# Kernel tuning notes

Hardware: AMD Instinct MI355X
Metric: run time of the kernel (lower is better)

## Reference

```python
import jax, jax.numpy as jnp
import numpy as np

C = 128
EPS = 1e-5


def _ln(x, g, b):
    m = jnp.mean(x, axis=-1, keepdims=True)
    v = jnp.mean((x - m) ** 2, axis=-1, keepdims=True)
    return (x - m) * jax.lax.rsqrt(v + EPS) * g + b


def setup_inputs() -> dict:
    key = jax.random.key(0)
    ks = jax.random.split(key, 10)
    B, N = 1, 384
    s = 1.0 / np.sqrt(C)
    inp = {
        "z": jax.random.normal(ks[0], (B, N, N, C), dtype=jnp.float32),
        "ln1_g": jnp.ones((C,), jnp.float32),
        "ln1_b": jnp.zeros((C,), jnp.float32),
        "ln2_g": jnp.ones((C,), jnp.float32),
        "ln2_b": jnp.zeros((C,), jnp.float32),
        "Wa": jax.random.uniform(ks[1], (C, C), jnp.float32, -s, s),
        "ba": jnp.zeros((C,), jnp.float32),
        "Wga": jax.random.uniform(ks[2], (C, C), jnp.float32, -s, s),
        "bga": jnp.zeros((C,), jnp.float32),
        "Wb": jax.random.uniform(ks[3], (C, C), jnp.float32, -s, s),
        "bb": jnp.zeros((C,), jnp.float32),
        "Wgb": jax.random.uniform(ks[4], (C, C), jnp.float32, -s, s),
        "bgb": jnp.zeros((C,), jnp.float32),
        "Wg": jax.random.uniform(ks[5], (C, C), jnp.float32, -s, s),
        "bg": jnp.zeros((C,), jnp.float32),
        "Wo": jax.random.uniform(ks[6], (C, C), jnp.float32, -s, s),
        "bo": jnp.zeros((C,), jnp.float32),
    }
    return inp


def reference(z, ln1_g, ln1_b, ln2_g, ln2_b, Wa, ba, Wga, bga, Wb, bb, Wgb, bgb, Wg, bg, Wo, bo):
    # z: (B, i, j, c)
    zn = _ln(z, ln1_g, ln1_b)
    a = (zn @ Wa + ba) * jax.nn.sigmoid(zn @ Wga + bga)      # (B,i,k,c)
    b = (zn @ Wb + bb) * jax.nn.sigmoid(zn @ Wgb + bgb)      # (B,j,k,c)
    gate = jax.nn.sigmoid(zn @ Wg + bg)                      # (B,i,j,c)
    o = jnp.einsum('bikc,bjkc->bijc', a, b)                  # outgoing triangle update
    return gate * (_ln(o, ln2_g, ln2_b) @ Wo + bo)
```

## Files before the change

### kernel.cpp

```cpp
#include <hip/hip_runtime.h>
#include <stdint.h>

typedef _Float16 f16x8 __attribute__((ext_vector_type(8)));
typedef float floatx4 __attribute__((ext_vector_type(4)));
typedef unsigned int u32x4 __attribute__((ext_vector_type(4)));

#define RR 147456
#define NC 128
#define NN 384

__device__ inline floatx4 zero4() { floatx4 v; v[0]=0.f; v[1]=0.f; v[2]=0.f; v[3]=0.f; return v; }
__device__ inline float sigmoidf_(float x) { return 1.f / (1.f + __expf(-x)); }

__global__ __launch_bounds__(256) void k0_wt(
    const float* __restrict__ w0, const float* __restrict__ w1,
    const float* __restrict__ w2, const float* __restrict__ w3,
    const float* __restrict__ w4, const float* __restrict__ w5,
    _Float16* __restrict__ wf)
{
  const float* w;
  switch (blockIdx.x) {
    case 0: w = w0; break; case 1: w = w1; break; case 2: w = w2; break;
    case 3: w = w3; break; case 4: w = w4; break; default: w = w5; break;
  }
  _Float16* out = wf + blockIdx.x * 16384;
  const int t = threadIdx.x;
  for (int it = 0; it < 64; ++it) {
    int f = it * 256 + t;
    int j  = f & 7;
    int ln = (f >> 3) & 63;
    int nt = (f >> 9) & 7;
    int k0 = f >> 12;
    int k = k0 * 32 + (ln >> 4) * 8 + j;
    int n = nt * 16 + (ln & 15);
    out[f] = (_Float16)w[k * 128 + n];
  }
}

__global__ __launch_bounds__(256, 4) void k2_ln_gemm(
    const float* __restrict__ z, const float* __restrict__ ln1g, const float* __restrict__ ln1b,
    const _Float16* __restrict__ wf,
    const float* __restrict__ ba, const float* __restrict__ bga,
    const float* __restrict__ bb, const float* __restrict__ bgb,
    const float* __restrict__ bg,
    _Float16* __restrict__ at, _Float16* __restrict__ bt, _Float16* __restrict__ gate)
{
  __shared__ __align__(16) _Float16 zns[64][136];
  __shared__ __align__(16) _Float16 bnc[4][32 * 72];
  const int t = threadIdx.x;
  const int w = t >> 6, lane = t & 63;
  const int l15 = lane & 15, quad = lane >> 4;
  const int r0 = blockIdx.x * 64;
  const int nt0 = w * 2;

  {
    const int g = lane >> 4, h = lane & 15;
    float4 ga = *(const float4*)(ln1g + h*8);
    float4 gb = *(const float4*)(ln1g + h*8 + 4);
    float4 bba = *(const float4*)(ln1b + h*8);
    float4 bbb = *(const float4*)(ln1b + h*8 + 4);
    #pragma unroll
    for (int rr = 0; rr < 4; ++rr) {
      int row = w * 16 + rr * 4 + g;
      const float* zp = z + (size_t)(r0 + row) * NC + h * 8;
      float4 xa = *(const float4*)zp;
      float4 xb = *(const float4*)(zp + 4);
      float s = xa.x + xa.y + xa.z + xa.w + xb.x + xb.y + xb.z + xb.w;
      float q = xa.x*xa.x + xa.y*xa.y + xa.z*xa.z + xa.w*xa.w
              + xb.x*xb.x + xb.y*xb.y + xb.z*xb.z + xb.w*xb.w;
      #pragma unroll
      for (int m = 1; m < 16; m <<= 1) { s += __shfl_xor(s, m); q += __shfl_xor(q, m); }
      float mean = s * (1.f/128.f);
      float var  = q * (1.f/128.f) - mean*mean;
      float rs = rsqrtf(var + 1e-5f);
      union { uint4 u; _Float16 hh[8]; } pk;
      pk.hh[0] = (_Float16)((xa.x - mean) * rs * ga.x + bba.x);
      pk.hh[1] = (_Float16)((xa.y - mean) * rs * ga.y + bba.y);
      pk.hh[2] = (_Float16)((xa.z - mean) * rs * ga.z + bba.z);
      pk.hh[3] = (_Float16)((xa.w - mean) * rs * ga.w + bba.w);
      pk.hh[4] = (_Float16)((xb.x - mean) * rs * gb.x + bbb.x);
      pk.hh[5] = (_Float16)((xb.y - mean) * rs * gb.y + bbb.y);
      pk.hh[6] = (_Float16)((xb.z - mean) * rs * gb.z + bbb.z);
      pk.hh[7] = (_Float16)((xb.w - mean) * rs * gb.w + bbb.w);
      *(uint4*)&zns[row][h * 8] = pk.u;
    }
  }
  __syncthreads();

  const _Float16* pw = wf + lane * 8;
  f16x8 bw[4][2];
  floatx4 acc[4][2];
  union PkU { unsigned int u; _Float16 h[2]; };
  PkU sig[4][2][2];

  auto loadw = [&](int slot) {
    const _Float16* p = pw + slot * 16384;
    #pragma unroll
    for (int k0 = 0; k0 < 4; ++k0)
      #pragma unroll
      for (int j = 0; j < 2; ++j)
        bw[k0][j] = *(const f16x8*)(p + (k0*8 + nt0 + j) * 512);
  };
  auto dogemm = [&]() {
    #pragma unroll
    for (int mt = 0; mt < 4; ++mt) {
      acc[mt][0] = zero4(); acc[mt][1] = zero4();
      #pragma unroll
      for (int k0 = 0; k0 < 4; ++k0) {
        f16x8 af = *(const f16x8*)&zns[mt*16 + l15][k0*32 + quad*8];
        acc[mt][0] = __builtin_amdgcn_mfma_f32_16x16x32_f16(af, bw[k0][0], acc[mt][0], 0, 0, 0);
        acc[mt][1] = __builtin_amdgcn_mfma_f32_16x16x32_f16(af, bw[k0][1], acc[mt][1], 0, 0, 0);
      }
    }
  };
  auto sigpack = [&](const float* big) {
    #pragma unroll
    for (int j = 0; j < 2; ++j) {
      float bgv = big[(nt0 + j)*16 + l15];
      #pragma unroll
      for (int mt = 0; mt < 4; ++mt) {
        sig[mt][j][0].h[0] = (_Float16)sigmoidf_(acc[mt][j][0] + bgv);
        sig[mt][j][0].h[1] = (_Float16)sigmoidf_(acc[mt][j][1] + bgv);
        sig[mt][j][1].h[0] = (_Float16)sigmoidf_(acc[mt][j][2] + bgv);
        sig[mt][j][1].h[1] = (_Float16)sigmoidf_(acc[mt][j][3] + bgv);
      }
    }
  };
  auto bounce_out = [&](_Float16* dst) {
    asm volatile("s_waitcnt lgkmcnt(0)" ::: "memory");
    _Float16* base = dst + (size_t)blockIdx.x * 8192 + w * 2048;
    #pragma unroll
    for (int i = 0; i < 4; ++i) {
      int f = i * 512 + lane * 8;
      int cp = f >> 6, pos = f & 63;
      u32x4 v = *(const u32x4*)&bnc[w][cp * 72 + pos];
      __builtin_nontemporal_store(v, (u32x4*)(base + f));
    }
  };
  auto combine_store = [&](const float* bia, _Float16* dst) {
    #pragma unroll
    for (int j = 0; j < 2; ++j) {
      int c = (nt0 + j)*16 + l15;
      float bav = bia[c];
      #pragma unroll
      for (int mt = 0; mt < 4; ++mt) {
        union { uint2 u2; _Float16 h[4]; } pk;
        pk.h[0] = (_Float16)((acc[mt][j][0] + bav) * (float)sig[mt][j][0].h[0]);
        pk.h[1] = (_Float16)((acc[mt][j][1] + bav) * (float)sig[mt][j][0].h[1]);
        pk.h[2] = (_Float16)((acc[mt][j][2] + bav) * (float)sig[mt][j][1].h[0]);
        pk.h[3] = (_Float16)((acc[mt][j][3] + bav) * (float)sig[mt][j][1].h[1]);
        *(uint2*)&bnc[w][(j*16 + l15) * 72 + mt*16 + quad*4] = pk.u2;
      }
    }
    bounce_out(dst);
  };

  loadw(1); dogemm(); sigpack(bga);
  loadw(0); dogemm();
  loadw(3);
  combine_store(ba, at);
  dogemm(); sigpack(bgb);
  loadw(2); dogemm();
  loadw(4);
  combine_store(bb, bt);
  dogemm();
  #pragma unroll
  for (int j = 0; j < 2; ++j) {
    float bgv = bg[(nt0 + j)*16 + l15];
    #pragma unroll
    for (int mt = 0; mt < 4; ++mt) {
      union { uint2 u2; _Float16 h[4]; } pk;
      #pragma unroll
      for (int r = 0; r < 4; ++r)
        pk.h[r] = (_Float16)sigmoidf_(acc[mt][j][r] + bgv);
      *(uint2*)&bnc[w][(j*16 + l15) * 72 + mt*16 + quad*4] = pk.u2;
    }
  }
  bounce_out(gate);
}

__global__ __launch_bounds__(128, 2) void k3_tri(
    const _Float16* __restrict__ at, const _Float16* __restrict__ bt, _Float16* __restrict__ o)
{
  __shared__ __align__(16) _Float16 As[2][128 * 40];
  __shared__ __align__(16) _Float16 Bs[2][128 * 40];
  const int t = threadIdx.x;
  const int w = t >> 6, lane = t & 63, l15 = lane & 15, quad = lane >> 4;
  const int c = blockIdx.y;
  const int i0 = (blockIdx.x / 3) * 128, j0 = (blockIdx.x % 3) * 128;

  const int sj = (t & 3) * 8, sr = t >> 2;
  f16x8 aS[4], bS[4];

  auto gload = [&](int kk) {
    size_t ko = ((size_t)(kk >> 6)) * 8192 + (size_t)((kk & 63) + sj) + (size_t)c * 64;
    #pragma unroll
    for (int s2 = 0; s2 < 4; ++s2) {
      int row = s2 * 32 + sr;
      aS[s2] = *(const f16x8*)(at + (size_t)(i0 + row) * 6 * 8192 + ko);
      bS[s2] = *(const f16x8*)(bt + (size_t)(j0 + row) * 6 * 8192 + ko);
    }
  };
  auto swrite = [&](int buf) {
    #pragma unroll
    for (int s2 = 0; s2 < 4; ++s2) {
      int row = s2 * 32 + sr;
      *(f16x8*)&As[buf][row * 40 + sj] = aS[s2];
      *(f16x8*)&Bs[buf][row * 40 + sj] = bS[s2];
    }
  };

  floatx4 acc[4][8];
  #pragma unroll
  for (int mt = 0; mt < 4; ++mt)
    #pragma unroll
    for (int nt = 0; nt < 8; ++nt) acc[mt][nt] = zero4();

  auto compute = [&](int buf) {
    f16x8 af[4], bfr[8];
    #pragma unroll
    for (int mt = 0; mt < 4; ++mt)
      af[mt] = *(const f16x8*)&As[buf][(w*64 + mt*16 + l15) * 40 + quad*8];
    #pragma unroll
    for (int nt = 0; nt < 8; ++nt)
      bfr[nt] = *(const f16x8*)&Bs[buf][(nt*16 + l15) * 40 + quad*8];
    #pragma unroll
    for (int mt = 0; mt < 4; ++mt)
      #pragma unroll
      for (int nt = 0; nt < 8; ++nt)
        acc[mt][nt] = __builtin_amdgcn_mfma_f32_16x16x32_f16(af[mt], bfr[nt], acc[mt][nt], 0, 0, 0);
  };

  gload(0); swrite(0); __syncthreads();
  for (int s = 0; s < 12; ++s) {
    if (s + 1 < 12) gload((s + 1) * 32);
    compute(s & 1);
    if (s + 1 < 12) { swrite((s + 1) & 1); __syncthreads(); }
  }

  #pragma unroll
  for (int mt = 0; mt < 4; ++mt) {
    #pragma unroll
    for (int r = 0; r < 4; ++r) {
      int i = i0 + w*64 + mt*16 + quad*4 + r;
      _Float16* ob = o + (size_t)(i*6 + (j0 >> 6)) * 8192 + (size_t)c * 64;
      #pragma unroll
      for (int nt = 0; nt < 8; ++nt) {
        _Float16* p = ob + (size_t)(nt >> 2) * 8192 + (nt & 3)*16 + l15;
        __builtin_nontemporal_store((_Float16)acc[mt][nt][r], p);
      }
    }
  }
}

__global__ __launch_bounds__(256, 4) void k4_out(
    const _Float16* __restrict__ o, const _Float16* __restrict__ gate,
    const float* __restrict__ ln2g, const float* __restrict__ ln2b,
    const _Float16* __restrict__ wo5, const float* __restrict__ bo,
    float* __restrict__ out)
{
  __shared__ __align__(16) _Float16 osb[64][136];
  const int t = threadIdx.x;
  const int w = t >> 6, lane = t & 63, l15 = lane & 15, quad = lane >> 4;
  const int r0 = blockIdx.x * 64;
  const int nt0 = w * 2;

  {
    const _Float16* ob = o + (size_t)blockIdx.x * 8192;
    #pragma unroll
    for (int it = 0; it < 4; ++it) {
      int f = (it * 256 + t) * 8;
      int cx = f >> 6, p = f & 63;
      f16x8 v = *(const f16x8*)(ob + f);
      #pragma unroll
      for (int i = 0; i < 8; ++i) osb[p + i][cx] = v[i];
    }
  }
  __syncthreads();

  {
    const int g = lane >> 4, h = lane & 15;
    float4 ga = *(const float4*)(ln2g + h*8);
    float4 gb = *(const float4*)(ln2g + h*8 + 4);
    float4 bba = *(const float4*)(ln2b + h*8);
    float4 bbb = *(const float4*)(ln2b + h*8 + 4);
    #pragma unroll
    for (int rr = 0; rr < 4; ++rr) {
      int row = w * 16 + rr * 4 + g;
      f16x8 xv = *(const f16x8*)&osb[row][h*8];
      float x0 = (float)xv[0], x1 = (float)xv[1], x2 = (float)xv[2], x3 = (float)xv[3];
      float x4 = (float)xv[4], x5 = (float)xv[5], x6 = (float)xv[6], x7 = (float)xv[7];
      float s = x0+x1+x2+x3+x4+x5+x6+x7;
      float q = x0*x0+x1*x1+x2*x2+x3*x3+x4*x4+x5*x5+x6*x6+x7*x7;
      #pragma unroll
      for (int m = 1; m < 16; m <<= 1) { s += __shfl_xor(s, m); q += __shfl_xor(q, m); }
      float mean = s * (1.f/128.f);
      float var  = q * (1.f/128.f) - mean*mean;
      float rs = rsqrtf(var + 1e-5f);
      union { uint4 u; _Float16 hh[8]; } pk;
      pk.hh[0] = (_Float16)((x0 - mean) * rs * ga.x + bba.x);
      pk.hh[1] = (_Float16)((x1 - mean) * rs * ga.y + bba.y);
      pk.hh[2] = (_Float16)((x2 - mean) * rs * ga.z + bba.z);
      pk.hh[3] = (_Float16)((x3 - mean) * rs * ga.w + bba.w);
      pk.hh[4] = (_Float16)((x4 - mean) * rs * gb.x + bbb.x);
      pk.hh[5] = (_Float16)((x5 - mean) * rs * gb.y + bbb.y);
      pk.hh[6] = (_Float16)((x6 - mean) * rs * gb.z + bbb.z);
      pk.hh[7] = (_Float16)((x7 - mean) * rs * gb.w + bbb.w);
      *(uint4*)&osb[row][h * 8] = pk.u;
    }
  }
  __syncthreads();

  f16x8 bw[4][2];
  {
    const _Float16* p = wo5 + lane * 8;
    #pragma unroll
    for (int k0 = 0; k0 < 4; ++k0)
      #pragma unroll
      for (int j = 0; j < 2; ++j)
        bw[k0][j] = *(const f16x8*)(p + (k0*8 + nt0 + j) * 512);
  }
  floatx4 acc[4][2];
  #pragma unroll
  for (int mt = 0; mt < 4; ++mt) {
    acc[mt][0] = zero4(); acc[mt][1] = zero4();
    #pragma unroll
    for (int k0 = 0; k0 < 4; ++k0) {
      f16x8 af = *(const f16x8*)&osb[mt*16 + l15][k0*32 + quad*8];
      acc[mt][0] = __builtin_amdgcn_mfma_f32_16x16x32_f16(af, bw[k0][0], acc[mt][0], 0, 0, 0);
      acc[mt][1] = __builtin_amdgcn_mfma_f32_16x16x32_f16(af, bw[k0][1], acc[mt][1], 0, 0, 0);
    }
  }

  #pragma unroll
  for (int j = 0; j < 2; ++j) {
    int cch = (nt0 + j)*16 + l15;
    float bov = bo[cch];
    #pragma unroll
    for (int mt = 0; mt < 4; ++mt) {
      union { uint2 u2; _Float16 h[4]; } gk;
      gk.u2 = *(const uint2*)(gate + (size_t)blockIdx.x * 8192 + (size_t)cch * 64 + mt*16 + quad*4);
      #pragma unroll
      for (int r = 0; r < 4; ++r) {
        int rl = mt*16 + quad*4 + r;
        __builtin_nontemporal_store((float)gk.h[r] * (acc[mt][j][r] + bov),
                                    out + (size_t)(r0 + rl) * NC + cch);
      }
    }
  }
}

extern "C" void kernel_launch(void* const* d_in, const int* in_sizes, int n_in,
                              void* d_out, int out_size, void* d_ws, size_t ws_size,
                              hipStream_t stream) {
  const float* z    = (const float*)d_in[0];
  const float* l1g  = (const float*)d_in[1];
  const float* l1b  = (const float*)d_in[2];
  const float* l2g  = (const float*)d_in[3];
  const float* l2b  = (const float*)d_in[4];
  const float* Wa   = (const float*)d_in[5];
  const float* ba   = (const float*)d_in[6];
  const float* Wga  = (const float*)d_in[7];
  const float* bga  = (const float*)d_in[8];
  const float* Wb   = (const float*)d_in[9];
  const float* bb   = (const float*)d_in[10];
  const float* Wgb  = (const float*)d_in[11];
  const float* bgb  = (const float*)d_in[12];
  const float* Wg   = (const float*)d_in[13];
  const float* bg   = (const float*)d_in[14];
  const float* Wo   = (const float*)d_in[15];
  const float* bo   = (const float*)d_in[16];

  char* ws = (char*)d_ws;
  _Float16* at_  = (_Float16*)(ws + 0);
  _Float16* bt_  = (_Float16*)(ws + 37748736);
  _Float16* gate = (_Float16*)(ws + 75497472);
  _Float16* o16  = (_Float16*)(ws + 113246208);
  _Float16* wf   = (_Float16*)(ws + 188743680);

  hipLaunchKernelGGL(k0_wt, dim3(6), dim3(256), 0, stream, Wa, Wga, Wb, Wgb, Wg, Wo, wf);
  hipLaunchKernelGGL(k2_ln_gemm, dim3(2304), dim3(256), 0, stream,
                     z, l1g, l1b, wf, ba, bga, bb, bgb, bg, at_, bt_, gate);
  hipLaunchKernelGGL(k3_tri, dim3(9, 128), dim3(128), 0, stream, at_, bt_, o16);
  hipLaunchKernelGGL(k4_out, dim3(2304), dim3(256), 0, stream,
                     o16, gate, l2g, l2b, wf + 5*16384, bo, (float*)d_out);
}
```

Baseline: 335.9 us.

## Double-buffer weight fragments, remap triangle grid per XCD, prefetch gate loads

The LN+GEMM kernel now keeps two register sets of weight fragments, so the next weight slot loads while the current GEMM runs. Its occupancy hint drops from 4 to 3 waves to leave room for the extra registers. The triangle kernel flattens its grid and maps block IDs so that all 9 tiles of one channel land on the same XCD, aiming for better L2 reuse of the at/bt slices. The output kernel issues its weight and gate loads before the LayerNorm phase so their latency overlaps that work, at the cost of more live registers.

```diff
diff --git a/kernel.cpp b/kernel.cpp
--- a/kernel.cpp
+++ b/kernel.cpp
@@ -37,7 +37,7 @@
   }
 }
 
-__global__ __launch_bounds__(256, 4) void k2_ln_gemm(
+__global__ __launch_bounds__(256, 3) void k2_ln_gemm(
     const float* __restrict__ z, const float* __restrict__ ln1g, const float* __restrict__ ln1b,
     const _Float16* __restrict__ wf,
     const float* __restrict__ ba, const float* __restrict__ bga,
@@ -88,12 +88,12 @@
   __syncthreads();
 
   const _Float16* pw = wf + lane * 8;
-  f16x8 bw[4][2];
+  f16x8 bwA[4][2], bwB[4][2];
   floatx4 acc[4][2];
   union PkU { unsigned int u; _Float16 h[2]; };
   PkU sig[4][2][2];
 
-  auto loadw = [&](int slot) {
+  auto loadw = [&](f16x8 (&bw)[4][2], int slot) {
     const _Float16* p = pw + slot * 16384;
     #pragma unroll
     for (int k0 = 0; k0 < 4; ++k0)
@@ -101,7 +101,7 @@
       for (int j = 0; j < 2; ++j)
         bw[k0][j] = *(const f16x8*)(p + (k0*8 + nt0 + j) * 512);
   };
-  auto dogemm = [&]() {
+  auto dogemm = [&](const f16x8 (&bw)[4][2]) {
     #pragma unroll
     for (int mt = 0; mt < 4; ++mt) {
       acc[mt][0] = zero4(); acc[mt][1] = zero4();
@@ -155,15 +155,15 @@
     bounce_out(dst);
   };
 
-  loadw(1); dogemm(); sigpack(bga);
-  loadw(0); dogemm();
-  loadw(3);
-  combine_store(ba, at);
-  dogemm(); sigpack(bgb);
-  loadw(2); dogemm();
-  loadw(4);
-  combine_store(bb, bt);
-  dogemm();
+  loadw(bwA, 1); loadw(bwB, 0);
+  dogemm(bwA); sigpack(bga);
+  loadw(bwA, 3);
+  dogemm(bwB); combine_store(ba, at);
+  loadw(bwB, 2);
+  dogemm(bwA); sigpack(bgb);
+  loadw(bwA, 4);
+  dogemm(bwB); combine_store(bb, bt);
+  dogemm(bwA);
   #pragma unroll
   for (int j = 0; j < 2; ++j) {
     float bgv = bg[(nt0 + j)*16 + l15];
@@ -186,8 +186,12 @@
   __shared__ __align__(16) _Float16 Bs[2][128 * 40];
   const int t = threadIdx.x;
   const int w = t >> 6, lane = t & 63, l15 = lane & 15, quad = lane >> 4;
-  const int c = blockIdx.y;
-  const int i0 = (blockIdx.x / 3) * 128, j0 = (blockIdx.x % 3) * 128;
+
+  const int b = blockIdx.x;
+  const int xcd = b & 7, kk9 = b >> 3;
+  const int c = xcd + 8 * (kk9 / 9);
+  const int tile = kk9 % 9;
+  const int i0 = (tile / 3) * 128, j0 = (tile % 3) * 128;
 
   const int sj = (t & 3) * 8, sr = t >> 2;
   f16x8 aS[4], bS[4];
@@ -264,6 +268,25 @@
   const int w = t >> 6, lane = t & 63, l15 = lane & 15, quad = lane >> 4;
   const int r0 = blockIdx.x * 64;
   const int nt0 = w * 2;
+
+  f16x8 bw[4][2];
+  {
+    const _Float16* p = wo5 + lane * 8;
+    #pragma unroll
+    for (int k0 = 0; k0 < 4; ++k0)
+      #pragma unroll
+      for (int j = 0; j < 2; ++j)
+        bw[k0][j] = *(const f16x8*)(p + (k0*8 + nt0 + j) * 512);
+  }
+  union GkU { uint2 u2; _Float16 h[4]; };
+  GkU gk[2][4];
+  #pragma unroll
+  for (int j = 0; j < 2; ++j) {
+    int cch = (nt0 + j)*16 + l15;
+    #pragma unroll
+    for (int mt = 0; mt < 4; ++mt)
+      gk[j][mt].u2 = *(const uint2*)(gate + (size_t)blockIdx.x * 8192 + (size_t)cch * 64 + mt*16 + quad*4);
+  }
 
   {
     const _Float16* ob = o + (size_t)blockIdx.x * 8192;
@@ -311,15 +334,6 @@
   }
   __syncthreads();
 
-  f16x8 bw[4][2];
-  {
-    const _Float16* p = wo5 + lane * 8;
-    #pragma unroll
-    for (int k0 = 0; k0 < 4; ++k0)
-      #pragma unroll
-      for (int j = 0; j < 2; ++j)
-        bw[k0][j] = *(const f16x8*)(p + (k0*8 + nt0 + j) * 512);
-  }
   floatx4 acc[4][2];
   #pragma unroll
   for (int mt = 0; mt < 4; ++mt) {
@@ -338,12 +352,10 @@
     float bov = bo[cch];
     #pragma unroll
     for (int mt = 0; mt < 4; ++mt) {
-      union { uint2 u2; _Float16 h[4]; } gk;
-      gk.u2 = *(const uint2*)(gate + (size_t)blockIdx.x * 8192 + (size_t)cch * 64 + mt*16 + quad*4);
       #pragma unroll
       for (int r = 0; r < 4; ++r) {
         int rl = mt*16 + quad*4 + r;
-        __builtin_nontemporal_store((float)gk.h[r] * (acc[mt][j][r] + bov),
+        __builtin_nontemporal_store((float)gk[j][mt].h[r] * (acc[mt][j][r] + bov),
                                     out + (size_t)(r0 + rl) * NC + cch);
       }
     }
@@ -381,7 +393,7 @@
   hipLaunchKernelGGL(k0_wt, dim3(6), dim3(256), 0, stream, Wa, Wga, Wb, Wgb, Wg, Wo, wf);
   hipLaunchKernelGGL(k2_ln_gemm, dim3(2304), dim3(256), 0, stream,
                      z, l1g, l1b, wf, ba, bga, bb, bgb, bg, at_, bt_, gate);
-  hipLaunchKernelGGL(k3_tri, dim3(9, 128), dim3(128), 0, stream, at_, bt_, o16);
+  hipLaunchKernelGGL(k3_tri, dim3(1152), dim3(128), 0, stream, at_, bt_, o16);
   hipLaunchKernelGGL(k4_out, dim3(2304), dim3(256), 0, stream,
                      o16, gate, l2g, l2b, wf + 5*16384, bo, (float*)d_out);
 }
```

Measured after the change: 310.4 us. -7.6%, faster.
